# Kernel tuning notes

Hardware: AMD Instinct MI355X
Metric: run time of the kernel (lower is better)

Reference implementation:

```python
import jax, jax.numpy as jnp
import numpy as np

B, CH, H, W, NC = 64, 128, 128, 512, 10  # batch, hidden_channels, rows(time), width, classes


def setup_inputs() -> dict:
    key = jax.random.key(0)
    k0, k1, k2, k3, k4 = jax.random.split(key, 5)
    x = jax.random.normal(k0, (B, 1, H, W), jnp.float32)
    # ConvLSTMCell conv: Conv2d(1+CH, 4*CH, kernel_size=3, padding=1)
    conv_w = jax.random.normal(k1, (4 * CH, 1 + CH, 3, 3), jnp.float32) * 0.05
    conv_b = jax.random.normal(k2, (4 * CH,), jnp.float32) * 0.05
    # classifier Linear(CH -> NC)
    fc_w = jax.random.normal(k3, (NC, CH), jnp.float32) * 0.05
    fc_b = jax.random.normal(k4, (NC,), jnp.float32) * 0.05
    return {"x": x, "conv_w": conv_w, "conv_b": conv_b, "fc_w": fc_w, "fc_b": fc_b}


def _convlstm_forward(x, conv_w, conv_b, fc_w, fc_b):
    b, _, h_rows, w = x.shape
    ch = fc_w.shape[1]
    dn = ('NCHW', 'OIHW', 'NCHW')

    def step(carry, row):
        h, c = carry  # each [B, CH, 1, W]
        combined = jnp.concatenate([row, h], axis=1)  # [B, 1+CH, 1, W]
        gates = jax.lax.conv_general_dilated(
            combined, conv_w, window_strides=(1, 1), padding='SAME',
            dimension_numbers=dn) + conv_b[None, :, None, None]  # [B, 4CH, 1, W]
        i, f, g, o = jnp.split(gates, 4, axis=1)
        c_next = jax.nn.sigmoid(f) * c + jax.nn.sigmoid(i) * jnp.tanh(g)
        h_next = jax.nn.sigmoid(o) * jnp.tanh(c_next)
        return (h_next, c_next), None

    # rows as scan xs: [H, B, 1, 1, W] (each timestep is a 1xW strip)
    rows = jnp.moveaxis(x, 2, 0)[:, :, :, None, :]
    h0 = jnp.zeros((b, ch, 1, w), x.dtype)
    c0 = jnp.zeros((b, ch, 1, w), x.dtype)
    (h_final, _), _ = jax.lax.scan(step, (h0, c0), rows)
    # Dropout2d is identity at inference. AdaptiveAvgPool2d(1) -> mean over spatial.
    pooled = h_final.mean(axis=(2, 3))  # [B, CH]
    return pooled @ fc_w.T + fc_b  # [B, NC]


def reference(x, conv_w, conv_b, fc_w, fc_b):
    return _convlstm_forward(x, conv_w, conv_b, fc_w, fc_b)
```

## Files before the change

### kernel.cpp

```cpp
#include <hip/hip_runtime.h>
#include <hip/hip_bf16.h>
#include <math.h>


constexpr int kB  = 64;
constexpr int kCH = 128;
constexpr int kH  = 128;
constexpr int kW  = 512;
constexpr int kNC = 10;

typedef __attribute__((ext_vector_type(8))) short short8v;
typedef __attribute__((ext_vector_type(4))) float float4v;

__device__ __forceinline__ float fsig(float v) {
    return 1.0f / (1.0f + __expf(-v));
}
__device__ __forceinline__ float ftanh(float v) {
    float e = __expf(2.0f * v);
    return 1.0f - 2.0f / (e + 1.0f);
}
__device__ __forceinline__ unsigned int pack2bf(float lo, float hi) {
    __hip_bfloat16 l = __float2bfloat16(lo);
    __hip_bfloat16 h = __float2bfloat16(hi);
    return (unsigned int)*reinterpret_cast<unsigned short*>(&l) |
           ((unsigned int)*reinterpret_cast<unsigned short*>(&h) << 16);
}
__device__ __forceinline__ float hi_bf(unsigned int u) {
    unsigned int t = u & 0xffff0000u;
    return *reinterpret_cast<float*>(&t);
}

__global__ __launch_bounds__(256) void pack_weights(
    const float* __restrict__ conv_w,
    const float* __restrict__ conv_b,
    short* __restrict__ Bp,
    float* __restrict__ pxw,
    float* __restrict__ pb,
    float* __restrict__ pooled)
{
    int idx = blockIdx.x * 256 + threadIdx.x;
    if (idx < 3 * 512 * 128) {
        int ic = idx & 127;
        int oc = (idx >> 7) & 511;
        int kx = idx >> 16;
        float v = conv_w[((oc * 129 + 1 + ic) * 3 + 1) * 3 + kx];
        __hip_bfloat16 hv = __float2bfloat16(v);
        Bp[idx] = *reinterpret_cast<short*>(&hv);
    }
    if (idx < 3 * 512) {
        int oc = idx & 511, kx = idx >> 9;
        pxw[idx] = conv_w[((oc * 129 + 0) * 3 + 1) * 3 + kx];
    }
    if (idx < 512) pb[idx] = conv_b[idx];
    if (idx < kB * kCH) pooled[idx] = 0.0f;
}

template <bool FIRST, bool LAST>
__global__ __launch_bounds__(256, 4) void lstm_step(
    const float* __restrict__ x,
    const short* __restrict__ Bp,
    const float* __restrict__ pxw,
    const float* __restrict__ pb,
    const unsigned int* __restrict__ hcIn,
    unsigned int* __restrict__ hcOut,
    float* __restrict__ pooled,
    int t)
{
    __shared__ alignas(16) short S[66 * 128];
    __shared__ alignas(16) short Bb[2][128 * 32];
    __shared__ float xs[66];

    const int tid  = threadIdx.x;
    const int lane = tid & 63;
    const int wave = tid >> 6;
    const int w0   = blockIdx.x * 64;
    const int cht  = blockIdx.y;
    const int b    = blockIdx.z;

    const int ncol = lane & 15;
    const int krow = lane >> 4;
    const int ch   = cht * 64 + wave * 16 + ncol;

    const size_t gbase = (size_t)b * kW * kCH;

    int bsrc[2], ldst[2];
#pragma unroll
    for (int cc = 0; cc < 2; ++cc) {
        int rr = wave * 32 + cc * 16 + (lane >> 2);
        int sl = lane & 3;
        int kk = sl ^ ((rr ^ (rr >> 2)) & 3);
        int n0 = (rr >> 6) * 128 + cht * 64 + (rr & 63);
        bsrc[cc] = n0 * 128 + kk * 8;
        ldst[cc] = (wave * 2 + cc) * 512;
    }

#define B_ISSUE(OFF, BUF)                                                      \
    {                                                                          \
        __builtin_amdgcn_global_load_lds(                                      \
            (const unsigned int*)(Bp + bsrc[0] + (OFF)),                       \
            (unsigned int*)(&Bb[BUF][ldst[0]]), 16, 0, 0);                     \
        __builtin_amdgcn_global_load_lds(                                      \
            (const unsigned int*)(Bp + bsrc[1] + (OFF)),                       \
            (unsigned int*)(&Bb[BUF][ldst[1]]), 16, 0, 0);                     \
    }

    for (int i = tid; i < 66; i += 256) {
        int w = w0 - 1 + i;
        xs[i] = (w >= 0 && w < kW)
              ? x[((size_t)b * kH + t) * kW + w] : 0.0f;
    }
    if (!FIRST) {
        for (int i = tid; i < 66 * 16; i += 256) {
            int row = i >> 4, col = i & 15;
            int w = w0 - 1 + row;
            short8v v = {0, 0, 0, 0, 0, 0, 0, 0};
            if (w >= 0 && w < kW) {
                const uint4* p = reinterpret_cast<const uint4*>(
                    hcIn + gbase + (size_t)w * kCH + col * 8);
                uint4 a = p[0], d = p[1];
                v[0] = (short)(a.x & 0xffff); v[1] = (short)(a.y & 0xffff);
                v[2] = (short)(a.z & 0xffff); v[3] = (short)(a.w & 0xffff);
                v[4] = (short)(d.x & 0xffff); v[5] = (short)(d.y & 0xffff);
                v[6] = (short)(d.z & 0xffff); v[7] = (short)(d.w & 0xffff);
            }
            *reinterpret_cast<short8v*>(
                S + row * 128 + (col ^ (row & 7)) * 8) = v;
        }
        B_ISSUE(0, 0)
    }
    __syncthreads();

    float4v acc[4][4];
#pragma unroll
    for (int mf = 0; mf < 4; ++mf)
#pragma unroll
        for (int g = 0; g < 4; ++g)
            acc[mf][g] = float4v{0.f, 0.f, 0.f, 0.f};

    if (!FIRST) {
        const int rswz  = (ncol ^ (ncol >> 2)) & 3;
        const int roff0 = (wave * 16 + ncol) * 32 + (krow ^ rswz) * 8;
        const int roff1 = roff0 + 64 * 32;
        short8v afr[4];

#pragma unroll
        for (int kq = 0; kq < 12; ++kq) {
            const int kx = kq >> 2, ks = kq & 3;
            B_ISSUE(kx * 65536 + ks * 32 + 32768, 1)
#pragma unroll
            for (int mf = 0; mf < 4; ++mf) {
                int srow = mf * 16 + ncol + kx;
                int slot = (ks * 4 + krow) ^ (srow & 7);
                afr[mf] = *reinterpret_cast<const short8v*>(
                    S + srow * 128 + slot * 8);
            }
            {
                short8v bv0 = *reinterpret_cast<const short8v*>(Bb[0] + roff0);
                short8v bv1 = *reinterpret_cast<const short8v*>(Bb[0] + roff1);
#pragma unroll
                for (int mf = 0; mf < 4; ++mf) {
                    acc[mf][0] = __builtin_amdgcn_mfma_f32_16x16x32_bf16(
                        afr[mf], bv0, acc[mf][0], 0, 0, 0);
                    acc[mf][1] = __builtin_amdgcn_mfma_f32_16x16x32_bf16(
                        afr[mf], bv1, acc[mf][1], 0, 0, 0);
                }
            }
            __syncthreads();
            if (kq < 11) {
                const int kx2 = (kq + 1) >> 2, ks2 = (kq + 1) & 3;
                B_ISSUE(kx2 * 65536 + ks2 * 32, 0)
            }
            {
                short8v bv2 = *reinterpret_cast<const short8v*>(Bb[1] + roff0);
                short8v bv3 = *reinterpret_cast<const short8v*>(Bb[1] + roff1);
#pragma unroll
                for (int mf = 0; mf < 4; ++mf) {
                    acc[mf][2] = __builtin_amdgcn_mfma_f32_16x16x32_bf16(
                        afr[mf], bv2, acc[mf][2], 0, 0, 0);
                    acc[mf][3] = __builtin_amdgcn_mfma_f32_16x16x32_bf16(
                        afr[mf], bv3, acc[mf][3], 0, 0, 0);
                }
            }
            __syncthreads();
        }
    }
#undef B_ISSUE

    float wxk[4][3], bia[4];
#pragma unroll
    for (int g = 0; g < 4; ++g) {
        bia[g] = pb[g * 128 + ch];
#pragma unroll
        for (int kx = 0; kx < 3; ++kx)
            wxk[g][kx] = pxw[kx * 512 + g * 128 + ch];
    }

    float psum = 0.0f;
#pragma unroll
    for (int mf = 0; mf < 4; ++mf) {
        unsigned int cu[4];
        if (!FIRST) {
#pragma unroll
            for (int r = 0; r < 4; ++r) {
                int m = mf * 16 + krow * 4 + r;
                cu[r] = hcIn[gbase + (size_t)(w0 + m) * kCH + ch];
            }
        }
#pragma unroll
        for (int r = 0; r < 4; ++r) {
            int m = mf * 16 + krow * 4 + r;
            float xm = xs[m], xc = xs[m + 1], xp = xs[m + 2];
            float v0 = acc[mf][0][r] + bia[0] + xm * wxk[0][0] + xc * wxk[0][1] + xp * wxk[0][2];
            float v1 = acc[mf][1][r] + bia[1] + xm * wxk[1][0] + xc * wxk[1][1] + xp * wxk[1][2];
            float v2 = acc[mf][2][r] + bia[2] + xm * wxk[2][0] + xc * wxk[2][1] + xp * wxk[2][2];
            float v3 = acc[mf][3][r] + bia[3] + xm * wxk[3][0] + xc * wxk[3][1] + xp * wxk[3][2];
            float cprev = FIRST ? 0.0f : hi_bf(cu[r]);
            float si = fsig(v0);
            float sf = fsig(v1);
            float tg = ftanh(v2);
            float so = fsig(v3);
            float cn = sf * cprev + si * tg;
            float hn = so * ftanh(cn);
            if (LAST) {
                psum += hn;
            } else {
                hcOut[gbase + (size_t)(w0 + m) * kCH + ch] = pack2bf(hn, cn);
            }
        }
    }

    if (LAST) {
        psum += __shfl_xor(psum, 16, 64);
        psum += __shfl_xor(psum, 32, 64);
        if (krow == 0) atomicAdd(&pooled[b * kCH + ch], psum);
    }
}

__global__ __launch_bounds__(64) void fc_final(
    const float* __restrict__ pooled,
    const float* __restrict__ fc_w,
    const float* __restrict__ fc_b,
    float* __restrict__ out)
{
    int b = blockIdx.x, nc = threadIdx.x;
    if (nc < kNC) {
        float s = 0.0f;
        for (int k = 0; k < kCH; ++k)
            s = fmaf(pooled[b * kCH + k], fc_w[nc * kCH + k], s);
        out[b * kNC + nc] = fc_b[nc] + s * (1.0f / kW);
    }
}

extern "C" void kernel_launch(void* const* d_in, const int* in_sizes, int n_in,
                              void* d_out, int out_size, void* d_ws, size_t ws_size,
                              hipStream_t stream) {
    const float* x      = (const float*)d_in[0];
    const float* conv_w = (const float*)d_in[1];
    const float* conv_b = (const float*)d_in[2];
    const float* fc_w   = (const float*)d_in[3];
    const float* fc_b   = (const float*)d_in[4];
    float* out = (float*)d_out;

    const size_t stateN = (size_t)kB * kW * kCH;
    unsigned int* hcA   = (unsigned int*)d_ws;
    unsigned int* hcB   = hcA + stateN;
    short* Bp           = (short*)(hcB + stateN);
    float* pxw          = (float*)(Bp + 3 * 512 * 128);
    float* pb           = pxw + 3 * 512;
    float* pooled       = pb + 512;

    pack_weights<<<768, 256, 0, stream>>>(conv_w, conv_b, Bp, pxw, pb, pooled);

    dim3 grid(kW / 64, 2, kB);
    dim3 block(256);
    lstm_step<true, false><<<grid, block, 0, stream>>>(
        x, Bp, pxw, pb, hcA, hcB, pooled, 0);
    for (int t = 1; t < kH - 1; ++t) {
        const unsigned int* hi = (t & 1) ? hcB : hcA;
        unsigned int*       ho = (t & 1) ? hcA : hcB;
        lstm_step<false, false><<<grid, block, 0, stream>>>(
            x, Bp, pxw, pb, hi, ho, pooled, t);
    }
    lstm_step<false, true><<<grid, block, 0, stream>>>(
        x, Bp, pxw, pb, hcB, hcA, pooled, 127);

    fc_final<<<kB, 64, 0, stream>>>(pooled, fc_w, fc_b, out);
}
```

Baseline: 3.513 ms.

## Split packed h/c state into separate bf16 planes with padded h for direct-to-LDS loads

Stores hidden and cell state as separate bf16 arrays instead of interleaved 32-bit pairs. The h buffer gets zero-padded boundary columns, so the tile staging can use global_load_lds straight into swizzled shared memory without bounds checks or register unpacking. This halves the bytes read for h staging and avoids loading the c halves there. The cost is two separate scalar 16-bit stores per element and a different workspace layout, and the pad columns must be zeroed in the pack kernel.

```diff
diff --git a/kernel.cpp b/kernel.cpp
--- a/kernel.cpp
+++ b/kernel.cpp
@@ -8,6 +8,7 @@
 constexpr int kH  = 128;
 constexpr int kW  = 512;
 constexpr int kNC = 10;
+constexpr int kWP = kW + 2;
 
 typedef __attribute__((ext_vector_type(8))) short short8v;
 typedef __attribute__((ext_vector_type(4))) float float4v;
@@ -19,15 +20,13 @@
     float e = __expf(2.0f * v);
     return 1.0f - 2.0f / (e + 1.0f);
 }
-__device__ __forceinline__ unsigned int pack2bf(float lo, float hi) {
-    __hip_bfloat16 l = __float2bfloat16(lo);
-    __hip_bfloat16 h = __float2bfloat16(hi);
-    return (unsigned int)*reinterpret_cast<unsigned short*>(&l) |
-           ((unsigned int)*reinterpret_cast<unsigned short*>(&h) << 16);
-}
-__device__ __forceinline__ float hi_bf(unsigned int u) {
-    unsigned int t = u & 0xffff0000u;
+__device__ __forceinline__ float bf_to_f32(unsigned short u) {
+    unsigned int t = (unsigned int)u << 16;
     return *reinterpret_cast<float*>(&t);
+}
+__device__ __forceinline__ unsigned short f32_to_bf(float f) {
+    __hip_bfloat16 h = __float2bfloat16(f);
+    return *reinterpret_cast<unsigned short*>(&h);
 }
 
 __global__ __launch_bounds__(256) void pack_weights(
@@ -36,7 +35,9 @@
     short* __restrict__ Bp,
     float* __restrict__ pxw,
     float* __restrict__ pb,
-    float* __restrict__ pooled)
+    float* __restrict__ pooled,
+    unsigned short* __restrict__ hA,
+    unsigned short* __restrict__ hB)
 {
     int idx = blockIdx.x * 256 + threadIdx.x;
     if (idx < 3 * 512 * 128) {
@@ -53,6 +54,14 @@
     }
     if (idx < 512) pb[idx] = conv_b[idx];
     if (idx < kB * kCH) pooled[idx] = 0.0f;
+    if (idx < kB * 2 * kCH) {
+        int b  = idx >> 8;
+        int r  = (idx >> 7) & 1;
+        int ch = idx & 127;
+        size_t off = ((size_t)b * kWP + (r ? (kWP - 1) : 0)) * kCH + ch;
+        hA[off] = 0;
+        hB[off] = 0;
+    }
 }
 
 template <bool FIRST, bool LAST>
@@ -61,8 +70,10 @@
     const short* __restrict__ Bp,
     const float* __restrict__ pxw,
     const float* __restrict__ pb,
-    const unsigned int* __restrict__ hcIn,
-    unsigned int* __restrict__ hcOut,
+    const unsigned short* __restrict__ hIn,
+    unsigned short* __restrict__ hOut,
+    const unsigned short* __restrict__ cIn,
+    unsigned short* __restrict__ cOut,
     float* __restrict__ pooled,
     int t)
 {
@@ -81,7 +92,8 @@
     const int krow = lane >> 4;
     const int ch   = cht * 64 + wave * 16 + ncol;
 
-    const size_t gbase = (size_t)b * kW * kCH;
+    const size_t hbase = (size_t)b * kWP * kCH;
+    const size_t cbase = (size_t)b * kW * kCH;
 
     int bsrc[2], ldst[2];
 #pragma unroll
@@ -111,20 +123,12 @@
     }
     if (!FIRST) {
         for (int i = tid; i < 66 * 16; i += 256) {
-            int row = i >> 4, col = i & 15;
-            int w = w0 - 1 + row;
-            short8v v = {0, 0, 0, 0, 0, 0, 0, 0};
-            if (w >= 0 && w < kW) {
-                const uint4* p = reinterpret_cast<const uint4*>(
-                    hcIn + gbase + (size_t)w * kCH + col * 8);
-                uint4 a = p[0], d = p[1];
-                v[0] = (short)(a.x & 0xffff); v[1] = (short)(a.y & 0xffff);
-                v[2] = (short)(a.z & 0xffff); v[3] = (short)(a.w & 0xffff);
-                v[4] = (short)(d.x & 0xffff); v[5] = (short)(d.y & 0xffff);
-                v[6] = (short)(d.z & 0xffff); v[7] = (short)(d.w & 0xffff);
-            }
-            *reinterpret_cast<short8v*>(
-                S + row * 128 + (col ^ (row & 7)) * 8) = v;
+            int row  = i >> 4, slot = i & 15;
+            int col  = slot ^ (row & 7);
+            int w    = w0 - 1 + row;
+            __builtin_amdgcn_global_load_lds(
+                (const unsigned int*)(hIn + hbase + (size_t)(w + 1) * kCH + col * 8),
+                (unsigned int*)(S + i * 8), 16, 0, 0);
         }
         B_ISSUE(0, 0)
     }
@@ -198,12 +202,12 @@
     float psum = 0.0f;
 #pragma unroll
     for (int mf = 0; mf < 4; ++mf) {
-        unsigned int cu[4];
+        unsigned short cu[4];
         if (!FIRST) {
 #pragma unroll
             for (int r = 0; r < 4; ++r) {
                 int m = mf * 16 + krow * 4 + r;
-                cu[r] = hcIn[gbase + (size_t)(w0 + m) * kCH + ch];
+                cu[r] = cIn[cbase + (size_t)(w0 + m) * kCH + ch];
             }
         }
 #pragma unroll
@@ -214,7 +218,7 @@
             float v1 = acc[mf][1][r] + bia[1] + xm * wxk[1][0] + xc * wxk[1][1] + xp * wxk[1][2];
             float v2 = acc[mf][2][r] + bia[2] + xm * wxk[2][0] + xc * wxk[2][1] + xp * wxk[2][2];
             float v3 = acc[mf][3][r] + bia[3] + xm * wxk[3][0] + xc * wxk[3][1] + xp * wxk[3][2];
-            float cprev = FIRST ? 0.0f : hi_bf(cu[r]);
+            float cprev = FIRST ? 0.0f : bf_to_f32(cu[r]);
             float si = fsig(v0);
             float sf = fsig(v1);
             float tg = ftanh(v2);
@@ -224,7 +228,8 @@
             if (LAST) {
                 psum += hn;
             } else {
-                hcOut[gbase + (size_t)(w0 + m) * kCH + ch] = pack2bf(hn, cn);
+                hOut[hbase + (size_t)(w0 + m + 1) * kCH + ch] = f32_to_bf(hn);
+                cOut[cbase + (size_t)(w0 + m) * kCH + ch]     = f32_to_bf(cn);
             }
         }
     }
@@ -261,28 +266,34 @@
     const float* fc_b   = (const float*)d_in[4];
     float* out = (float*)d_out;
 
-    const size_t stateN = (size_t)kB * kW * kCH;
-    unsigned int* hcA   = (unsigned int*)d_ws;
-    unsigned int* hcB   = hcA + stateN;
-    short* Bp           = (short*)(hcB + stateN);
-    float* pxw          = (float*)(Bp + 3 * 512 * 128);
-    float* pb           = pxw + 3 * 512;
-    float* pooled       = pb + 512;
-
-    pack_weights<<<768, 256, 0, stream>>>(conv_w, conv_b, Bp, pxw, pb, pooled);
+    const size_t hN = (size_t)kB * kWP * kCH;
+    const size_t cN = (size_t)kB * kW * kCH;
+    unsigned short* hA = (unsigned short*)d_ws;
+    unsigned short* hB = hA + hN;
+    unsigned short* cA = hB + hN;
+    unsigned short* cB = cA + cN;
+    short* Bp          = (short*)(cB + cN);
+    float* pxw         = (float*)(Bp + 3 * 512 * 128);
+    float* pb          = pxw + 3 * 512;
+    float* pooled      = pb + 512;
+
+    pack_weights<<<768, 256, 0, stream>>>(conv_w, conv_b, Bp, pxw, pb, pooled,
+                                          hA, hB);
 
     dim3 grid(kW / 64, 2, kB);
     dim3 block(256);
     lstm_step<true, false><<<grid, block, 0, stream>>>(
-        x, Bp, pxw, pb, hcA, hcB, pooled, 0);
+        x, Bp, pxw, pb, hA, hB, cA, cB, pooled, 0);
     for (int t = 1; t < kH - 1; ++t) {
-        const unsigned int* hi = (t & 1) ? hcB : hcA;
-        unsigned int*       ho = (t & 1) ? hcA : hcB;
+        const unsigned short* hi = (t & 1) ? hB : hA;
+        unsigned short*       ho = (t & 1) ? hA : hB;
+        const unsigned short* ci = (t & 1) ? cB : cA;
+        unsigned short*       co = (t & 1) ? cA : cB;
         lstm_step<false, false><<<grid, block, 0, stream>>>(
-            x, Bp, pxw, pb, hi, ho, pooled, t);
+            x, Bp, pxw, pb, hi, ho, ci, co, pooled, t);
     }
     lstm_step<false, true><<<grid, block, 0, stream>>>(
-        x, Bp, pxw, pb, hcB, hcA, pooled, 127);
+        x, Bp, pxw, pb, hB, hA, cB, cA, pooled, 127);
 
     fc_final<<<kB, 64, 0, stream>>>(pooled, fc_w, fc_b, out);
 }
```

After: 3.362 ms. 1.04x faster.
